# Performance work log

Hardware: AMD Instinct MI355X
Metric: run time of the kernel (lower is better)

## Reference

```python
import jax, jax.numpy as jnp
import numpy as np

NUM_ROUTE_NODES = 1152
IN_CHANNELS = 8
OUT_CHANNELS = 16
NUM_DIGITS = 10
NUM_ITERATIONS = 3
BATCH = 256


def squash(x):
    # Faithful to the original: uses the GLOBAL norm of the whole tensor,
    # not a per-capsule norm.
    norm = jnp.linalg.norm(x)
    sq = norm * norm
    return (sq / (1.0 + sq)) * (x / norm)


def setup_inputs() -> dict:
    key = jax.random.key(0)
    k_u, k_w = jax.random.split(key)
    u = jax.random.normal(k_u, (BATCH, NUM_ROUTE_NODES, IN_CHANNELS), dtype=jnp.float32)
    # W: (1, R, D, out, in) as in nn.Parameter(torch.randn(...))
    W = jax.random.normal(k_w, (1, NUM_ROUTE_NODES, NUM_DIGITS, OUT_CHANNELS, IN_CHANNELS), dtype=jnp.float32)
    return {"u": u, "W": W}


def reference(u, W):
    # u_hat[b,r,d,o] = sum_i W[0,r,d,o,i] * u[b,r,i]
    u_hat = jnp.einsum('rdoi,bri->brdo', W[0], u)  # (B, R, D, O)
    R, D = u_hat.shape[1], u_hat.shape[2]
    b = jnp.zeros((R, D), dtype=u_hat.dtype)
    v = None
    for _ in range(NUM_ITERATIONS):
        c = jax.nn.softmax(b, axis=1)[None, :, :, None]     # (1, R, D, 1)
        s = jnp.sum(u_hat * c, axis=1)                      # (B, D, O)
        v = squash(s)                                       # (B, D, O)
        # agreement: a[b,r,d] = sum_o u_hat[b,r,d,o] * v[b,d,o]
        a = jnp.einsum('brdo,bdo->brd', u_hat, v)           # (B, R, D)
        b = b + jnp.sum(a, axis=0)                          # (R, D)
    return v
```

## Files before the change

### kernel.cpp

```cpp
#include <hip/hip_runtime.h>
#include <math.h>

#define R_NODES 1152
#define DIGITS 10
#define OUT_CH 16
#define IN_CH 8
#define BATCH 256
#define COLS 160
#define W_PER_R 1280
#define MROW 9216
#define NSPLIT 72
#define RPS 16
#define YB_S 8
#define UP 88
#define KST 264

typedef __attribute__((ext_vector_type(8))) short short8v;
typedef __attribute__((ext_vector_type(4))) float floatx4;

__device__ inline unsigned short f2bf(float x) {
    union { float f; unsigned int i; } v; v.f = x;
    unsigned int r = v.i + 0x7FFFu + ((v.i >> 16) & 1u);
    return (unsigned short)(r >> 16);
}
__device__ inline float bf2f(unsigned short x) {
    union { unsigned int i; float f; } v; v.i = ((unsigned int)x) << 16;
    return v.f;
}

__global__ __launch_bounds__(256, 3) void k_s(
    const float* __restrict__ u,
    const float* __restrict__ W,
    const float* __restrict__ blog,
    unsigned short* __restrict__ part,
    float* __restrict__ sqz,
    int nbuf)
{
    __shared__ unsigned short ulds[32 * UP];
    __shared__ unsigned short wlds[COLS * UP];
    __shared__ float cs[RPS * DIGITS];

    const int split = blockIdx.x;
    const int b0 = blockIdx.y * 32;
    const int t = threadIdx.x;
    const int r0 = split * RPS;

    if (split == 0 && blockIdx.y == 0 && t == 0) *sqz = 0.f;

    if (t < RPS * DIGITS) {
        cs[t] = nbuf ? blog[r0 * DIGITS + t] : 0.f;
    }
    __syncthreads();
    if (t < RPS) {
        float e[DIGITS];
        float m = -1e30f;
#pragma unroll
        for (int d = 0; d < DIGITS; ++d) m = fmaxf(m, cs[t*10 + d]);
        float ssum = 0.f;
#pragma unroll
        for (int d = 0; d < DIGITS; ++d) { e[d] = expf(cs[t*10 + d] - m); ssum += e[d]; }
        float inv = 1.f / ssum;
#pragma unroll
        for (int d = 0; d < DIGITS; ++d) cs[t*10 + d] = e[d] * inv;
    }
    __syncthreads();

    const int w = t >> 6, l = t & 63;
    const int mtile = w & 1;
    const int ncol0 = (w >> 1) * 5;
    const int koff = (l >> 4) * 8;
    const int arow = (mtile * 16 + (l & 15)) * UP;

    floatx4 acc[5];
#pragma unroll
    for (int j = 0; j < 5; ++j) acc[j] = (floatx4){0.f, 0.f, 0.f, 0.f};

    for (int ch = 0; ch < 2; ++ch) {
        const int rc = r0 + ch * 8;
        float4 uv[2];
#pragma unroll
        for (int p = 0; p < 2; ++p) {
            int idx = t + p * 256;
            int b = idx >> 4, q = idx & 15;
            uv[p] = *(const float4*)(u + (size_t)(b0 + b) * (R_NODES * IN_CH)
                                       + (size_t)rc * IN_CH + q * 4);
        }
        float4 wr[10];
        {
            const float4* Wg = (const float4*)(W + (size_t)rc * W_PER_R);
#pragma unroll
            for (int p = 0; p < 10; ++p) wr[p] = Wg[t + p * 256];
        }
        if (ch) __syncthreads();
#pragma unroll
        for (int p = 0; p < 2; ++p) {
            int idx = t + p * 256;
            int b = idx >> 4, q = idx & 15;
            *(short4*)&ulds[b * UP + q * 4] =
                make_short4((short)f2bf(uv[p].x), (short)f2bf(uv[p].y),
                            (short)f2bf(uv[p].z), (short)f2bf(uv[p].w));
        }
#pragma unroll
        for (int p = 0; p < 10; ++p) {
            int e4 = t + p * 256;
            int e  = e4 * 4;
            int r_l = e4 / 320;
            int rem = e - r_l * W_PER_R;
            int col = rem >> 3;
            int i0  = e & 7;
            float cv = cs[(ch * 8 + r_l) * 10 + (rem >> 7)];
            float4 w4 = wr[p];
            *(short4*)&wlds[col * UP + r_l * 8 + i0] =
                make_short4((short)f2bf(w4.x * cv), (short)f2bf(w4.y * cv),
                            (short)f2bf(w4.z * cv), (short)f2bf(w4.w * cv));
        }
        __syncthreads();
        short8v a0 = *(const short8v*)&ulds[arow + koff];
        short8v a1 = *(const short8v*)&ulds[arow + 32 + koff];
#pragma unroll
        for (int j = 0; j < 5; ++j) {
            const int bcol = ((ncol0 + j) * 16 + (l & 15)) * UP;
            short8v bb0 = *(const short8v*)&wlds[bcol + koff];
            short8v bb1 = *(const short8v*)&wlds[bcol + 32 + koff];
            acc[j] = __builtin_amdgcn_mfma_f32_16x16x32_bf16(a0, bb0, acc[j], 0, 0, 0);
            acc[j] = __builtin_amdgcn_mfma_f32_16x16x32_bf16(a1, bb1, acc[j], 0, 0, 0);
        }
    }

    unsigned short* pp = part + (size_t)split * (BATCH * COLS);
    const int gb = b0 + mtile * 16 + (l >> 4) * 4;
#pragma unroll
    for (int j = 0; j < 5; ++j) {
        const int gc = (ncol0 + j) * 16 + (l & 15);
#pragma unroll
        for (int reg = 0; reg < 4; ++reg)
            pp[(size_t)(gb + reg) * COLS + gc] = f2bf(acc[j][reg]);
    }
}

__global__ void k_sq(const unsigned short* __restrict__ part,
                     float* __restrict__ s,
                     float* __restrict__ sq)
{
    const int t = threadIdx.x;
    const int e0 = blockIdx.x * 64;
    const int el = t & 63, q = t >> 6;
    float v = 0.f;
    for (int sp = q; sp < NSPLIT; sp += 4)
        v += bf2f(part[(size_t)sp * (BATCH * COLS) + e0 + el]);
    __shared__ float red[256];
    red[t] = v;
    __syncthreads();
    if (t < 64) {
        float vv = red[t] + red[t + 64] + red[t + 128] + red[t + 192];
        s[e0 + t] = vv;
        float x = vv * vv;
#pragma unroll
        for (int off = 32; off > 0; off >>= 1)
            x += __shfl_down(x, off, 64);
        if (t == 0) atomicAdd(sq, x);
    }
}

__global__ __launch_bounds__(256, 3) void k_b(
    const float* __restrict__ u,
    const float* __restrict__ s,
    const float* __restrict__ W,
    const float* __restrict__ sqp,
    float* __restrict__ blog,
    int first)
{
    __shared__ unsigned short sld[16 * KST];
    __shared__ unsigned short uld[64 * KST];
    const int t = threadIdx.x;
    const int rig = blockIdx.x;
    const int d = blockIdx.y;

#pragma unroll
    for (int p = 0; p < 4; ++p) {
        int idx = t + p * 256;
        int b = idx >> 2, q = idx & 3;
        float4 v = *(const float4*)(s + (size_t)b * COLS + d * 16 + q * 4);
        sld[(q*4+0)*KST + b] = f2bf(v.x);
        sld[(q*4+1)*KST + b] = f2bf(v.y);
        sld[(q*4+2)*KST + b] = f2bf(v.z);
        sld[(q*4+3)*KST + b] = f2bf(v.w);
    }
#pragma unroll
    for (int p = 0; p < 16; ++p) {
        int idx = t + p * 256;
        int b = idx >> 4, q = idx & 15;
        float4 v = *(const float4*)(u + (size_t)b * MROW + rig * 64 + q * 4);
        uld[(q*4+0)*KST + b] = f2bf(v.x);
        uld[(q*4+1)*KST + b] = f2bf(v.y);
        uld[(q*4+2)*KST + b] = f2bf(v.z);
        uld[(q*4+3)*KST + b] = f2bf(v.w);
    }
    __syncthreads();

    const int w = t >> 6, l = t & 63;
    floatx4 acc = {0.f, 0.f, 0.f, 0.f};
#pragma unroll
    for (int ks = 0; ks < 8; ++ks) {
        int koff = ks * 32 + (l >> 4) * 8;
        short8v av = *(const short8v*)&sld[(l & 15) * KST + koff];
        short8v bv = *(const short8v*)&uld[(w * 16 + (l & 15)) * KST + koff];
        acc = __builtin_amdgcn_mfma_f32_16x16x32_bf16(av, bv, acc, 0, 0, 0);
    }

    const int r_l = 2 * w + ((l & 15) >> 3);
    const int r = rig * 8 + r_l;
    const float* Wp = W + (size_t)r * W_PER_R + d * 128 + (l & 7);
    float p = 0.f;
#pragma unroll
    for (int reg = 0; reg < 4; ++reg) {
        int o = (l >> 4) * 4 + reg;
        p = fmaf(Wp[o * 8], acc[reg], p);
    }
    p += __shfl_xor(p, 1, 64);
    p += __shfl_xor(p, 2, 64);
    p += __shfl_xor(p, 4, 64);
    p += __shfl_xor(p, 16, 64);
    p += __shfl_xor(p, 32, 64);

    if ((l & 55) == 0) {
        float q = *sqp;
        float scale = sqrtf(q) / (1.f + q);
        float prev = first ? 0.f : blog[r * DIGITS + d];
        blog[r * DIGITS + d] = prev + scale * p;
    }
}

__global__ void k_scale(const float* __restrict__ s,
                        const float* __restrict__ sq,
                        float* __restrict__ out)
{
    int e = blockIdx.x * 256 + threadIdx.x;
    float q = *sq;
    float scale = sqrtf(q) / (1.f + q);
    out[e] = s[e] * scale;
}

extern "C" void kernel_launch(void* const* d_in, const int* in_sizes, int n_in,
                              void* d_out, int out_size, void* d_ws, size_t ws_size,
                              hipStream_t stream)
{
    const float* u = (const float*)d_in[0];
    const float* W = (const float*)d_in[1];
    float* out = (float*)d_out;
    float* ws = (float*)d_ws;

    float* s     = ws;
    float* sqbuf = ws + 40960;
    float* blog  = ws + 41024;
    unsigned short* part = (unsigned short*)(ws + 41024 + 11520 + 64);

    for (int it = 0; it < 3; ++it) {
        k_s<<<dim3(NSPLIT, YB_S), dim3(256), 0, stream>>>(u, W, blog, part,
                                                          sqbuf + it, it);
        k_sq<<<dim3(BATCH * COLS / 64), dim3(256), 0, stream>>>(part, s, sqbuf + it);
        if (it < 2)
            k_b<<<dim3(144, 10), dim3(256), 0, stream>>>(u, s, W, sqbuf + it,
                                                         blog, it == 0 ? 1 : 0);
        else
            k_scale<<<dim3(BATCH * COLS / 256), dim3(256), 0, stream>>>(s, sqbuf + 2, out);
    }
}
```

Baseline: 104.1 us.

## Split agreement kernel over batch quarters and loop digits inside block

The agreement kernel now tiles over four batch quarters instead of ten digits. Each block loads its u slice once and loops over all ten digits, so the u tile is read and converted once per block rather than once per digit. The four batch quarters each write partial logits into their own buffer, and the routing kernel sums the four partials when it reads them. This trades repeated u loads for more barriers per block, more sequential MFMA work and four extra logit reads in the softmax step.

```diff
diff --git a/kernel.cpp b/kernel.cpp
--- a/kernel.cpp
+++ b/kernel.cpp
@@ -13,7 +13,8 @@
 #define RPS 16
 #define YB_S 8
 #define UP 88
-#define KST 264
+#define KB 72
+#define BLOG_N 11520
 
 typedef __attribute__((ext_vector_type(8))) short short8v;
 typedef __attribute__((ext_vector_type(4))) float floatx4;
@@ -31,7 +32,7 @@
 __global__ __launch_bounds__(256, 3) void k_s(
     const float* __restrict__ u,
     const float* __restrict__ W,
-    const float* __restrict__ blog,
+    const float* __restrict__ blog4,
     unsigned short* __restrict__ part,
     float* __restrict__ sqz,
     int nbuf)
@@ -48,7 +49,14 @@
     if (split == 0 && blockIdx.y == 0 && t == 0) *sqz = 0.f;
 
     if (t < RPS * DIGITS) {
-        cs[t] = nbuf ? blog[r0 * DIGITS + t] : 0.f;
+        float a = 0.f;
+        if (nbuf) {
+            a = blog4[r0 * DIGITS + t]
+              + blog4[BLOG_N + r0 * DIGITS + t]
+              + blog4[2 * BLOG_N + r0 * DIGITS + t]
+              + blog4[3 * BLOG_N + r0 * DIGITS + t];
+        }
+        cs[t] = a;
     }
     __syncthreads();
     if (t < RPS) {
@@ -167,67 +175,70 @@
     const float* __restrict__ s,
     const float* __restrict__ W,
     const float* __restrict__ sqp,
-    float* __restrict__ blog,
+    float* __restrict__ blog4,
     int first)
 {
-    __shared__ unsigned short sld[16 * KST];
-    __shared__ unsigned short uld[64 * KST];
+    __shared__ unsigned short uld[64 * KB];
+    __shared__ unsigned short sld[16 * KB];
     const int t = threadIdx.x;
     const int rig = blockIdx.x;
-    const int d = blockIdx.y;
+    const int bq = blockIdx.y;
+    const int b0 = bq * 64;
 
 #pragma unroll
     for (int p = 0; p < 4; ++p) {
         int idx = t + p * 256;
-        int b = idx >> 2, q = idx & 3;
-        float4 v = *(const float4*)(s + (size_t)b * COLS + d * 16 + q * 4);
-        sld[(q*4+0)*KST + b] = f2bf(v.x);
-        sld[(q*4+1)*KST + b] = f2bf(v.y);
-        sld[(q*4+2)*KST + b] = f2bf(v.z);
-        sld[(q*4+3)*KST + b] = f2bf(v.w);
-    }
-#pragma unroll
-    for (int p = 0; p < 16; ++p) {
-        int idx = t + p * 256;
         int b = idx >> 4, q = idx & 15;
-        float4 v = *(const float4*)(u + (size_t)b * MROW + rig * 64 + q * 4);
-        uld[(q*4+0)*KST + b] = f2bf(v.x);
-        uld[(q*4+1)*KST + b] = f2bf(v.y);
-        uld[(q*4+2)*KST + b] = f2bf(v.z);
-        uld[(q*4+3)*KST + b] = f2bf(v.w);
-    }
-    __syncthreads();
+        float4 v = *(const float4*)(u + (size_t)(b0 + b) * MROW + rig * 64 + q * 4);
+        uld[(q*4+0)*KB + b] = f2bf(v.x);
+        uld[(q*4+1)*KB + b] = f2bf(v.y);
+        uld[(q*4+2)*KB + b] = f2bf(v.z);
+        uld[(q*4+3)*KB + b] = f2bf(v.w);
+    }
 
     const int w = t >> 6, l = t & 63;
-    floatx4 acc = {0.f, 0.f, 0.f, 0.f};
-#pragma unroll
-    for (int ks = 0; ks < 8; ++ks) {
-        int koff = ks * 32 + (l >> 4) * 8;
-        short8v av = *(const short8v*)&sld[(l & 15) * KST + koff];
-        short8v bv = *(const short8v*)&uld[(w * 16 + (l & 15)) * KST + koff];
-        acc = __builtin_amdgcn_mfma_f32_16x16x32_bf16(av, bv, acc, 0, 0, 0);
-    }
-
+    const float q0 = *sqp;
+    const float scale = sqrtf(q0) / (1.f + q0);
     const int r_l = 2 * w + ((l & 15) >> 3);
     const int r = rig * 8 + r_l;
-    const float* Wp = W + (size_t)r * W_PER_R + d * 128 + (l & 7);
-    float p = 0.f;
-#pragma unroll
-    for (int reg = 0; reg < 4; ++reg) {
-        int o = (l >> 4) * 4 + reg;
-        p = fmaf(Wp[o * 8], acc[reg], p);
-    }
-    p += __shfl_xor(p, 1, 64);
-    p += __shfl_xor(p, 2, 64);
-    p += __shfl_xor(p, 4, 64);
-    p += __shfl_xor(p, 16, 64);
-    p += __shfl_xor(p, 32, 64);
-
-    if ((l & 55) == 0) {
-        float q = *sqp;
-        float scale = sqrtf(q) / (1.f + q);
-        float prev = first ? 0.f : blog[r * DIGITS + d];
-        blog[r * DIGITS + d] = prev + scale * p;
+    float* slot = blog4 + (size_t)bq * BLOG_N;
+
+    for (int d = 0; d < DIGITS; ++d) {
+        int sb = t >> 2, sq_ = t & 3;
+        float4 v = *(const float4*)(s + (size_t)(b0 + sb) * COLS + d * 16 + sq_ * 4);
+        if (d) __syncthreads();
+        sld[(sq_*4+0)*KB + sb] = f2bf(v.x);
+        sld[(sq_*4+1)*KB + sb] = f2bf(v.y);
+        sld[(sq_*4+2)*KB + sb] = f2bf(v.z);
+        sld[(sq_*4+3)*KB + sb] = f2bf(v.w);
+        __syncthreads();
+
+        floatx4 acc = {0.f, 0.f, 0.f, 0.f};
+#pragma unroll
+        for (int ks = 0; ks < 2; ++ks) {
+            int koff = ks * 32 + (l >> 4) * 8;
+            short8v av = *(const short8v*)&sld[(l & 15) * KB + koff];
+            short8v bv = *(const short8v*)&uld[(w * 16 + (l & 15)) * KB + koff];
+            acc = __builtin_amdgcn_mfma_f32_16x16x32_bf16(av, bv, acc, 0, 0, 0);
+        }
+
+        const float* Wp = W + (size_t)r * W_PER_R + d * 128 + (l & 7);
+        float p = 0.f;
+#pragma unroll
+        for (int reg = 0; reg < 4; ++reg) {
+            int o = (l >> 4) * 4 + reg;
+            p = fmaf(Wp[o * 8], acc[reg], p);
+        }
+        p += __shfl_xor(p, 1, 64);
+        p += __shfl_xor(p, 2, 64);
+        p += __shfl_xor(p, 4, 64);
+        p += __shfl_xor(p, 16, 64);
+        p += __shfl_xor(p, 32, 64);
+
+        if ((l & 55) == 0) {
+            float prev = first ? 0.f : slot[r * DIGITS + d];
+            slot[r * DIGITS + d] = prev + scale * p;
+        }
     }
 }
 
@@ -252,16 +263,16 @@
 
     float* s     = ws;
     float* sqbuf = ws + 40960;
-    float* blog  = ws + 41024;
-    unsigned short* part = (unsigned short*)(ws + 41024 + 11520 + 64);
+    float* blog4 = ws + 41024;
+    unsigned short* part = (unsigned short*)(ws + 41024 + 4 * BLOG_N + 64);
 
     for (int it = 0; it < 3; ++it) {
-        k_s<<<dim3(NSPLIT, YB_S), dim3(256), 0, stream>>>(u, W, blog, part,
+        k_s<<<dim3(NSPLIT, YB_S), dim3(256), 0, stream>>>(u, W, blog4, part,
                                                           sqbuf + it, it);
         k_sq<<<dim3(BATCH * COLS / 64), dim3(256), 0, stream>>>(part, s, sqbuf + it);
         if (it < 2)
-            k_b<<<dim3(144, 10), dim3(256), 0, stream>>>(u, s, W, sqbuf + it,
-                                                         blog, it == 0 ? 1 : 0);
+            k_b<<<dim3(144, 4), dim3(256), 0, stream>>>(u, s, W, sqbuf + it,
+                                                        blog4, it == 0 ? 1 : 0);
         else
             k_scale<<<dim3(BATCH * COLS / 256), dim3(256), 0, stream>>>(s, sqbuf + 2, out);
     }
```

New measurement: 95.98 us, median of 2. -7.8%, faster.
